# Kernel tuning notes

Hardware: AMD Instinct MI355X
Metric: run time of the kernel (lower is better)

Reference implementation:

```python
import jax, jax.numpy as jnp
import numpy as np

TOPK = 8
MIN_TEMP = 0.5
NEG = -1e9  # finite stand-in for -inf (same softmax result, safe grads)


def setup_inputs() -> dict:
    key = jax.random.key(0)
    ks = jax.random.split(key, 6)
    B, S, D, N, K = 4, 4096, 1024, 256, 8
    token_states = jax.random.normal(ks[0], (B, S, D), dtype=jnp.float32)
    set_states = jax.random.normal(ks[1], (B, N, D), dtype=jnp.float32)
    desc_router = jax.random.normal(ks[2], (N, D), dtype=jnp.float32)
    token_to_sets = jax.random.randint(ks[3], (S, K), 0, N)
    Wq = jax.random.normal(ks[4], (D, D), dtype=jnp.float32) / np.sqrt(D)
    bq = jnp.zeros((D,), dtype=jnp.float32)
    temperature = jnp.ones((1,), dtype=jnp.float32)
    return {"token_states": token_states, "set_states": set_states,
            "desc_router": desc_router, "token_to_sets": token_to_sets,
            "Wq": Wq, "bq": bq, "temperature": temperature}


def reference(token_states, set_states, desc_router, token_to_sets, Wq, bq, temperature):
    B, S, D = token_states.shape
    N = set_states.shape[1]
    scale = 1.0 / np.sqrt(D)

    # q = Linear(token_states)
    q = jnp.einsum('bsd,ed->bse', token_states, Wq) + bq
    scores = jnp.einsum('bse,ne->bsn', q, desc_router) * scale  # [B,S,N]

    # restrict_to_sets: boolean routing mask built by scatter
    rows = jnp.broadcast_to(jnp.arange(S)[:, None], token_to_sets.shape)
    cols = jnp.clip(token_to_sets, 0, N - 1)
    valid = token_to_sets >= 0
    mask = jnp.zeros((S, N), dtype=bool).at[rows, cols].max(valid)
    scores = jnp.where(mask[None], scores, NEG)

    # top-k keep (topk < num_sets)
    topk_scores, topk_idx = jax.lax.top_k(scores, TOPK)
    b_idx = jnp.arange(B)[:, None, None]
    s_idx = jnp.arange(S)[None, :, None]
    keep = jnp.full_like(scores, NEG).at[b_idx, s_idx, topk_idx].set(topk_scores)

    temp = jnp.maximum(temperature, MIN_TEMP)  # clamp(min=0.5)
    weights = jax.nn.softmax(keep / temp, axis=-1)  # [B,S,N]
    token_repr = jnp.einsum('bsn,bnd->bsd', weights, set_states)
    bank_indices = jnp.argmax(weights, axis=-1)
    return token_repr, bank_indices, weights, topk_idx
```

## Files before the change

### kernel.cpp

```cpp
#include <hip/hip_runtime.h>
#include <math.h>
#include <float.h>


namespace {
constexpr int kB = 4, kS = 4096, kD = 1024, kN = 256, kK = 8;
constexpr float kScale = 0.03125f;
constexpr float kNeg = -1e9f;
constexpr float kLog2e = 1.4426950408889634f;
constexpr size_t kBankOff = (size_t)kB * kS * kD;
constexpr size_t kWOff    = kBankOff + (size_t)kB * kS;
constexpr size_t kTopkOff = kWOff + (size_t)kB * kS * kN;
constexpr int kEC = 16;
constexpr int kEL = kD / kEC;
constexpr int kNT = kN / 8;
}

#if __has_builtin(__builtin_amdgcn_exp2f)
#define FAST_EXP2(x) __builtin_amdgcn_exp2f(x)
#else
#define FAST_EXP2(x) exp2f(x)
#endif
#if __has_builtin(__builtin_amdgcn_rcpf)
#define FAST_RCP(x) __builtin_amdgcn_rcpf(x)
#else
#define FAST_RCP(x) (1.0f / (x))
#endif

__global__ __launch_bounds__(256) void k_prep(const float* __restrict__ dr,
                                              const float* __restrict__ wq,
                                              float* __restrict__ part) {
  const int nt = blockIdx.x, ec = blockIdx.y, t = threadIdx.x;
  const float4* wq4 = reinterpret_cast<const float4*>(wq);
  float4 acc[8];
#pragma unroll
  for (int j = 0; j < 8; ++j) acc[j] = make_float4(0.f, 0.f, 0.f, 0.f);
  const int e0 = ec * kEL;
#pragma unroll 4
  for (int e = e0; e < e0 + kEL; ++e) {
    const float4 wv = wq4[(size_t)e * (kD / 4) + t];
#pragma unroll
    for (int j = 0; j < 8; ++j) {
      const float a = dr[(size_t)(nt * 8 + j) * kD + e];
      acc[j].x += a * wv.x; acc[j].y += a * wv.y;
      acc[j].z += a * wv.z; acc[j].w += a * wv.w;
    }
  }
  float4* p4 = reinterpret_cast<float4*>(part);
#pragma unroll
  for (int j = 0; j < 8; ++j)
    p4[((size_t)ec * kN + nt * 8 + j) * (kD / 4) + t] = acc[j];
}

__global__ __launch_bounds__(256) void k_reduce(const float* __restrict__ part,
                                                const float* __restrict__ dr,
                                                const float* __restrict__ bq,
                                                float* __restrict__ R,
                                                float* __restrict__ bias) {
  const int n = blockIdx.x, t = threadIdx.x;
  const float4* p4 = reinterpret_cast<const float4*>(part);
  float4 a = make_float4(0.f, 0.f, 0.f, 0.f);
#pragma unroll
  for (int ec = 0; ec < kEC; ++ec) {
    const float4 p = p4[((size_t)ec * kN + n) * (kD / 4) + t];
    a.x += p.x; a.y += p.y; a.z += p.z; a.w += p.w;
  }
  a.x *= kScale; a.y *= kScale; a.z *= kScale; a.w *= kScale;
  reinterpret_cast<float4*>(R)[(size_t)n * (kD / 4) + t] = a;

  if (t < 64) {
    const float4* b4 = reinterpret_cast<const float4*>(bq);
    const float4* dr4 = reinterpret_cast<const float4*>(dr + (size_t)n * kD);
    float p = 0.f;
#pragma unroll
    for (int i = 0; i < 4; ++i) {
      const float4 bb = b4[t * 4 + i];
      const float4 dd = dr4[t * 4 + i];
      p += bb.x * dd.x + bb.y * dd.y + bb.z * dd.z + bb.w * dd.w;
    }
#pragma unroll
    for (int off = 32; off; off >>= 1) p += __shfl_xor(p, off);
    if (t == 0) bias[n] = p * kScale;
  }
}

__global__ __launch_bounds__(256) void k_main(const float* __restrict__ ts,
                                              const float* __restrict__ ss,
                                              const int* __restrict__ t2s,
                                              const float* __restrict__ R,
                                              const float* __restrict__ bias,
                                              const float* __restrict__ temp_p,
                                              float* __restrict__ out) {
  const int lane = threadIdx.x & 63;
  const int wid = threadIdx.x >> 6;
  const int bid = blockIdx.x;
  const int xcd = bid & 7;
  const int b = xcd >> 1;
  int s_ = ((bid >> 3) << 2) + wid + ((xcd & 1) << 11);
  const int s = __builtin_amdgcn_readfirstlane(s_);
  const size_t row = (size_t)b * kS + s;

  int nraw[kK], nk[kK];
#pragma unroll
  for (int k = 0; k < kK; ++k) {
    nraw[k] = t2s[s * kK + k];
    const int n = nraw[k];
    nk[k] = n < 0 ? 0 : (n > kN - 1 ? kN - 1 : n);
  }
  int validmask = 0;
#pragma unroll
  for (int k = 0; k < kK; ++k) {
    bool v = (nraw[k] >= 0);
#pragma unroll
    for (int j = 0; j < kK; ++j)
      if (j < k && nk[j] == nk[k]) v = false;
    validmask |= v ? (1 << k) : 0;
  }
  const int cnt = __popc(validmask);

  const float4* ssb = reinterpret_cast<const float4*>(ss) + (size_t)b * kN * (kD / 4);
  float4 s0[kK];
#pragma unroll
  for (int k = 0; k < kK; ++k) s0[k] = ssb[(size_t)nk[k] * (kD / 4) + lane];

  const float4* t4 = reinterpret_cast<const float4*>(ts) + row * (kD / 4);
  const float4 tv0 = t4[lane];
  const float4 tv1 = t4[64 + lane];
  const float4 tv2 = t4[128 + lane];
  const float4 tv3 = t4[192 + lane];

  float pk[kK];
#pragma unroll
  for (int k = 0; k < kK; ++k) {
    const float4* r4 = reinterpret_cast<const float4*>(R) + (size_t)nk[k] * (kD / 4);
    const float4 r0 = r4[lane];
    const float4 r1 = r4[64 + lane];
    const float4 r2 = r4[128 + lane];
    const float4 r3 = r4[192 + lane];
    float a = tv0.x * r0.x + tv0.y * r0.y + tv0.z * r0.z + tv0.w * r0.w;
    a += tv1.x * r1.x + tv1.y * r1.y + tv1.z * r1.z + tv1.w * r1.w;
    a += tv2.x * r2.x + tv2.y * r2.y + tv2.z * r2.z + tv2.w * r2.w;
    a += tv3.x * r3.x + tv3.y * r3.y + tv3.z * r3.z + tv3.w * r3.w;
    pk[k] = a;
  }
#pragma unroll
  for (int k = 0; k < kK; ++k) {
    float a = pk[k];
    a += __shfl_xor(a, 1);
    a += __shfl_xor(a, 2);
    a += __shfl_xor(a, 4);
    a += __shfl_xor(a, 8);
    a += __shfl_xor(a, 16);
    a += __shfl_xor(a, 32);
    pk[k] = a + bias[nk[k]];
  }

  float mx = -INFINITY;
#pragma unroll
  for (int k = 0; k < kK; ++k)
    mx = fmaxf(mx, ((validmask >> k) & 1) ? pk[k] : -INFINITY);
  const float it = kLog2e * FAST_RCP(fmaxf(temp_p[0], 0.5f));
  float w[kK];
  float denom = 0.f;
#pragma unroll
  for (int k = 0; k < kK; ++k) {
    const float e = ((validmask >> k) & 1) ? FAST_EXP2((pk[k] - mx) * it) : 0.f;
    w[k] = e;
    denom += e;
  }
  const float rd = FAST_RCP(denom);
#pragma unroll
  for (int k = 0; k < kK; ++k) w[k] *= rd;

  float4* o4 = reinterpret_cast<float4*>(out) + row * (kD / 4);
  {
    float4 acc = make_float4(0.f, 0.f, 0.f, 0.f);
#pragma unroll
    for (int k = 0; k < kK; ++k) {
      acc.x += w[k] * s0[k].x; acc.y += w[k] * s0[k].y;
      acc.z += w[k] * s0[k].z; acc.w += w[k] * s0[k].w;
    }
    o4[lane] = acc;
  }
#pragma unroll
  for (int c = 1; c < 4; ++c) {
    float4 v[kK];
#pragma unroll
    for (int k = 0; k < kK; ++k)
      v[k] = ssb[(size_t)nk[k] * (kD / 4) + c * 64 + lane];
    float4 acc = make_float4(0.f, 0.f, 0.f, 0.f);
#pragma unroll
    for (int k = 0; k < kK; ++k) {
      acc.x += w[k] * v[k].x; acc.y += w[k] * v[k].y;
      acc.z += w[k] * v[k].z; acc.w += w[k] * v[k].w;
    }
    o4[c * 64 + lane] = acc;
  }

  {
    const int c0 = lane * 4;
    float4 wv = make_float4(0.f, 0.f, 0.f, 0.f);
#pragma unroll
    for (int k = 0; k < kK; ++k) {
      const bool vb = (validmask >> k) & 1;
      wv.x = (vb && nk[k] == c0    ) ? w[k] : wv.x;
      wv.y = (vb && nk[k] == c0 + 1) ? w[k] : wv.y;
      wv.z = (vb && nk[k] == c0 + 2) ? w[k] : wv.z;
      wv.w = (vb && nk[k] == c0 + 3) ? w[k] : wv.w;
    }
    reinterpret_cast<float4*>(out + kWOff)[row * (kN / 4) + lane] = wv;
  }

  unsigned long long pm0 = 0, pm1 = 0, pm2 = 0, pm3 = 0;
#pragma unroll
  for (int k = 0; k < kK; ++k) {
    const bool v = (validmask >> k) & 1;
    const unsigned long long bit = 1ull << (nk[k] & 63);
    const int wd = nk[k] >> 6;
    pm0 |= (v && wd == 0) ? bit : 0ull;
    pm1 |= (v && wd == 1) ? bit : 0ull;
    pm2 |= (v && wd == 2) ? bit : 0ull;
    pm3 |= (v && wd == 3) ? bit : 0ull;
  }
  int seq[kK];
#pragma unroll
  for (int i = 0; i < kK; ++i) {
    const unsigned long long i0 = ~pm0, i1 = ~pm1, i2 = ~pm2, i3 = ~pm3;
    const int c = i0 ? (__ffsll(i0) - 1)
                     : (i1 ? 64 + (__ffsll(i1) - 1)
                           : (i2 ? 128 + (__ffsll(i2) - 1)
                                 : 192 + (__ffsll(i3) - 1)));
    seq[i] = c;
    const unsigned long long b2 = 1ull << (c & 63);
    const int wd = c >> 6;
    pm0 |= (wd == 0) ? b2 : 0ull;
    pm1 |= (wd == 1) ? b2 : 0ull;
    pm2 |= (wd == 2) ? b2 : 0ull;
    pm3 |= (wd == 3) ? b2 : 0ull;
  }

  float fs[kK];
  int fi[kK];
#pragma unroll
  for (int k = 0; k < kK; ++k) {
    const bool v = (validmask >> k) & 1;
    const int jk = __popc((~validmask) & ((1 << k) - 1));
    int fv = seq[0];
#pragma unroll
    for (int j = 1; j < kK; ++j) fv = (jk == j) ? seq[j] : fv;
    fs[k] = v ? pk[k] : kNeg;
    fi[k] = v ? nk[k] : fv;
  }
#define CE(A, B)                                                        \
  {                                                                     \
    const bool sw = (fs[B] > fs[A]) || (fs[B] == fs[A] && fi[B] < fi[A]); \
    const float fa = fs[A], fb = fs[B];                                 \
    const int ia = fi[A], ib = fi[B];                                   \
    fs[A] = sw ? fb : fa; fs[B] = sw ? fa : fb;                         \
    fi[A] = sw ? ib : ia; fi[B] = sw ? ia : ib;                         \
  }
  CE(0,1) CE(2,3) CE(4,5) CE(6,7)
  CE(0,2) CE(1,3) CE(4,6) CE(5,7)
  CE(1,2) CE(5,6)
  CE(0,4) CE(1,5) CE(2,6) CE(3,7)
  CE(2,4) CE(3,5)
  CE(1,2) CE(3,4) CE(5,6)
#undef CE

  if (lane < kK) {
    int v = fi[0];
#pragma unroll
    for (int k = 1; k < kK; ++k) v = (lane == k) ? fi[k] : v;
    out[kTopkOff + row * kK + lane] = (float)v;
  }
  if (lane == 0) out[kBankOff + row] = (float)fi[0];
}

extern "C" void kernel_launch(void* const* d_in, const int* in_sizes, int n_in,
                              void* d_out, int out_size, void* d_ws, size_t ws_size,
                              hipStream_t stream) {
  const float* ts  = (const float*)d_in[0];
  const float* ss  = (const float*)d_in[1];
  const float* dr  = (const float*)d_in[2];
  const int*   t2s = (const int*)  d_in[3];
  const float* wq  = (const float*)d_in[4];
  const float* bq  = (const float*)d_in[5];
  const float* tmp = (const float*)d_in[6];
  float* out = (float*)d_out;

  float* R    = (float*)d_ws;
  float* bias = R + (size_t)kN * kD;
  float* part = out + kWOff;

  k_prep<<<dim3(kNT, kEC), 256, 0, stream>>>(dr, wq, part);
  k_reduce<<<kN, 256, 0, stream>>>(part, dr, bq, R, bias);
  k_main<<<kB * kS / 4, 256, 0, stream>>>(ts, ss, t2s, R, bias, tmp, out);
}
```

Measured before the change: 71.08 us.

## Share routed R rows across batches via LDS, one block per token

Remaps k_main so each block handles one sequence position and its four waves handle the four batches. Those waves share the same token_to_sets routing, so the eight projected router rows are loaded once into shared memory and reused instead of being re-read from global memory per batch. Also software-pipelines the set_states gathers in chunks, moves the weights store earlier, sets launch_bounds occupancy to 3 blocks, and halves the split count in the prep kernel. In exchange it adds a block barrier and 32KB of LDS per block, which may limit occupancy.

```diff
diff --git a/kernel.cpp b/kernel.cpp
--- a/kernel.cpp
+++ b/kernel.cpp
@@ -11,7 +11,7 @@
 constexpr size_t kBankOff = (size_t)kB * kS * kD;
 constexpr size_t kWOff    = kBankOff + (size_t)kB * kS;
 constexpr size_t kTopkOff = kWOff + (size_t)kB * kS * kN;
-constexpr int kEC = 16;
+constexpr int kEC = 8;
 constexpr int kEL = kD / kEC;
 constexpr int kNT = kN / 8;
 }
@@ -84,21 +84,19 @@
   }
 }
 
-__global__ __launch_bounds__(256) void k_main(const float* __restrict__ ts,
-                                              const float* __restrict__ ss,
-                                              const int* __restrict__ t2s,
-                                              const float* __restrict__ R,
-                                              const float* __restrict__ bias,
-                                              const float* __restrict__ temp_p,
-                                              float* __restrict__ out) {
+__global__ __launch_bounds__(256, 3) void k_main(const float* __restrict__ ts,
+                                                 const float* __restrict__ ss,
+                                                 const int* __restrict__ t2s,
+                                                 const float* __restrict__ R,
+                                                 const float* __restrict__ bias,
+                                                 const float* __restrict__ temp_p,
+                                                 float* __restrict__ out) {
   const int lane = threadIdx.x & 63;
-  const int wid = threadIdx.x >> 6;
+  const int wvb = threadIdx.x >> 6;
   const int bid = blockIdx.x;
-  const int xcd = bid & 7;
-  const int b = xcd >> 1;
-  int s_ = ((bid >> 3) << 2) + wid + ((xcd & 1) << 11);
-  const int s = __builtin_amdgcn_readfirstlane(s_);
-  const size_t row = (size_t)b * kS + s;
+  const int s = __builtin_amdgcn_readfirstlane(((bid & 7) << 9) | (bid >> 3));
+
+  __shared__ float4 lr[kK * 256];
 
   int nraw[kK], nk[kK];
 #pragma unroll
@@ -116,27 +114,41 @@
       if (j < k && nk[j] == nk[k]) v = false;
     validmask |= v ? (1 << k) : 0;
   }
-  const int cnt = __popc(validmask);
-
-  const float4* ssb = reinterpret_cast<const float4*>(ss) + (size_t)b * kN * (kD / 4);
-  float4 s0[kK];
-#pragma unroll
-  for (int k = 0; k < kK; ++k) s0[k] = ssb[(size_t)nk[k] * (kD / 4) + lane];
-
+
+  {
+    const int rk = threadIdx.x >> 5, rc = threadIdx.x & 31;
+    int myrow = nk[0];
+#pragma unroll
+    for (int k = 1; k < kK; ++k) myrow = (rk == k) ? nk[k] : myrow;
+    const float4* R4 = reinterpret_cast<const float4*>(R);
+#pragma unroll
+    for (int j = 0; j < 8; ++j)
+      lr[rk * 256 + rc + 32 * j] = R4[(size_t)myrow * 256 + rc + 32 * j];
+  }
+
+  const float4* ssb = reinterpret_cast<const float4*>(ss) + (size_t)wvb * kN * (kD / 4);
+  float4 c0[kK], c1[kK];
+#pragma unroll
+  for (int k = 0; k < kK; ++k) c0[k] = ssb[(size_t)nk[k] * (kD / 4) + lane];
+#pragma unroll
+  for (int k = 0; k < kK; ++k) c1[k] = ssb[(size_t)nk[k] * (kD / 4) + 64 + lane];
+
+  const size_t row = (size_t)wvb * kS + s;
   const float4* t4 = reinterpret_cast<const float4*>(ts) + row * (kD / 4);
   const float4 tv0 = t4[lane];
   const float4 tv1 = t4[64 + lane];
   const float4 tv2 = t4[128 + lane];
   const float4 tv3 = t4[192 + lane];
 
+  __syncthreads();
+
   float pk[kK];
 #pragma unroll
   for (int k = 0; k < kK; ++k) {
-    const float4* r4 = reinterpret_cast<const float4*>(R) + (size_t)nk[k] * (kD / 4);
-    const float4 r0 = r4[lane];
-    const float4 r1 = r4[64 + lane];
-    const float4 r2 = r4[128 + lane];
-    const float4 r3 = r4[192 + lane];
+    const float4 r0 = lr[k * 256 + lane];
+    const float4 r1 = lr[k * 256 + 64 + lane];
+    const float4 r2 = lr[k * 256 + 128 + lane];
+    const float4 r3 = lr[k * 256 + 192 + lane];
     float a = tv0.x * r0.x + tv0.y * r0.y + tv0.z * r0.z + tv0.w * r0.w;
     a += tv1.x * r1.x + tv1.y * r1.y + tv1.z * r1.z + tv1.w * r1.w;
     a += tv2.x * r2.x + tv2.y * r2.y + tv2.z * r2.z + tv2.w * r2.w;
@@ -172,43 +184,62 @@
 #pragma unroll
   for (int k = 0; k < kK; ++k) w[k] *= rd;
 
+  {
+    const int cb = lane * 4;
+    float4 wvv = make_float4(0.f, 0.f, 0.f, 0.f);
+#pragma unroll
+    for (int k = 0; k < kK; ++k) {
+      const bool vb = (validmask >> k) & 1;
+      wvv.x = (vb && nk[k] == cb    ) ? w[k] : wvv.x;
+      wvv.y = (vb && nk[k] == cb + 1) ? w[k] : wvv.y;
+      wvv.z = (vb && nk[k] == cb + 2) ? w[k] : wvv.z;
+      wvv.w = (vb && nk[k] == cb + 3) ? w[k] : wvv.w;
+    }
+    reinterpret_cast<float4*>(out + kWOff)[row * (kN / 4) + lane] = wvv;
+  }
+
   float4* o4 = reinterpret_cast<float4*>(out) + row * (kD / 4);
   {
     float4 acc = make_float4(0.f, 0.f, 0.f, 0.f);
 #pragma unroll
     for (int k = 0; k < kK; ++k) {
-      acc.x += w[k] * s0[k].x; acc.y += w[k] * s0[k].y;
-      acc.z += w[k] * s0[k].z; acc.w += w[k] * s0[k].w;
+      acc.x += w[k] * c0[k].x; acc.y += w[k] * c0[k].y;
+      acc.z += w[k] * c0[k].z; acc.w += w[k] * c0[k].w;
     }
     o4[lane] = acc;
   }
-#pragma unroll
-  for (int c = 1; c < 4; ++c) {
-    float4 v[kK];
-#pragma unroll
-    for (int k = 0; k < kK; ++k)
-      v[k] = ssb[(size_t)nk[k] * (kD / 4) + c * 64 + lane];
+  float4 c2[kK];
+#pragma unroll
+  for (int k = 0; k < kK; ++k) c2[k] = ssb[(size_t)nk[k] * (kD / 4) + 128 + lane];
+  {
     float4 acc = make_float4(0.f, 0.f, 0.f, 0.f);
 #pragma unroll
     for (int k = 0; k < kK; ++k) {
-      acc.x += w[k] * v[k].x; acc.y += w[k] * v[k].y;
-      acc.z += w[k] * v[k].z; acc.w += w[k] * v[k].w;
-    }
-    o4[c * 64 + lane] = acc;
-  }
-
-  {
-    const int c0 = lane * 4;
-    float4 wv = make_float4(0.f, 0.f, 0.f, 0.f);
-#pragma unroll
-    for (int k = 0; k < kK; ++k) {
-      const bool vb = (validmask >> k) & 1;
-      wv.x = (vb && nk[k] == c0    ) ? w[k] : wv.x;
-      wv.y = (vb && nk[k] == c0 + 1) ? w[k] : wv.y;
-      wv.z = (vb && nk[k] == c0 + 2) ? w[k] : wv.z;
-      wv.w = (vb && nk[k] == c0 + 3) ? w[k] : wv.w;
-    }
-    reinterpret_cast<float4*>(out + kWOff)[row * (kN / 4) + lane] = wv;
+      acc.x += w[k] * c1[k].x; acc.y += w[k] * c1[k].y;
+      acc.z += w[k] * c1[k].z; acc.w += w[k] * c1[k].w;
+    }
+    o4[64 + lane] = acc;
+  }
+  float4 c3[kK];
+#pragma unroll
+  for (int k = 0; k < kK; ++k) c3[k] = ssb[(size_t)nk[k] * (kD / 4) + 192 + lane];
+  {
+    float4 acc = make_float4(0.f, 0.f, 0.f, 0.f);
+#pragma unroll
+    for (int k = 0; k < kK; ++k) {
+      acc.x += w[k] * c2[k].x; acc.y += w[k] * c2[k].y;
+      acc.z += w[k] * c2[k].z; acc.w += w[k] * c2[k].w;
+    }
+    o4[128 + lane] = acc;
+  }
+  {
+    float4 acc = make_float4(0.f, 0.f, 0.f, 0.f);
+#pragma unroll
+    for (int k = 0; k < kK; ++k) {
+      acc.x += w[k] * c3[k].x; acc.y += w[k] * c3[k].y;
+      acc.z += w[k] * c3[k].z; acc.w += w[k] * c3[k].w;
+    }
+    o4[192 + lane] = acc;
   }
 
   unsigned long long pm0 = 0, pm1 = 0, pm2 = 0, pm3 = 0;
@@ -294,5 +325,5 @@
 
   k_prep<<<dim3(kNT, kEC), 256, 0, stream>>>(dr, wq, part);
   k_reduce<<<kN, 256, 0, stream>>>(part, dr, bq, R, bias);
-  k_main<<<kB * kS / 4, 256, 0, stream>>>(ts, ss, t2s, R, bias, tmp, out);
-}
+  k_main<<<kS, 256, 0, stream>>>(ts, ss, t2s, R, bias, tmp, out);
+}
```

New measurement: 87.14 us. +22.6%, slower.

## Split main kernel into scoring and weighted-gather kernels, halve prep split

Applied to the files above, without the earlier changes.

Splits the fused kernel into a scoring/top-k kernel that writes per-row weights and sorted indices to workspace, and a second kernel that gathers set_states and writes token_repr and the dense weights. This lowers register pressure in each kernel so more waves can hide memory latency. The softmax is now computed over the sorted top-k entries. It also halves the k_prep split factor. In exchange it adds a kernel launch and a small workspace round trip.

```diff
diff --git a/kernel.cpp b/kernel.cpp
--- a/kernel.cpp
+++ b/kernel.cpp
@@ -11,7 +11,7 @@
 constexpr size_t kBankOff = (size_t)kB * kS * kD;
 constexpr size_t kWOff    = kBankOff + (size_t)kB * kS;
 constexpr size_t kTopkOff = kWOff + (size_t)kB * kS * kN;
-constexpr int kEC = 16;
+constexpr int kEC = 8;
 constexpr int kEL = kD / kEC;
 constexpr int kNT = kN / 8;
 }
@@ -84,13 +84,13 @@
   }
 }
 
-__global__ __launch_bounds__(256) void k_main(const float* __restrict__ ts,
-                                              const float* __restrict__ ss,
-                                              const int* __restrict__ t2s,
-                                              const float* __restrict__ R,
-                                              const float* __restrict__ bias,
-                                              const float* __restrict__ temp_p,
-                                              float* __restrict__ out) {
+__global__ __launch_bounds__(256) void k_score(const float* __restrict__ ts,
+                                               const int* __restrict__ t2s,
+                                               const float* __restrict__ R,
+                                               const float* __restrict__ bias,
+                                               const float* __restrict__ temp_p,
+                                               int* __restrict__ st,
+                                               float* __restrict__ out) {
   const int lane = threadIdx.x & 63;
   const int wid = threadIdx.x >> 6;
   const int bid = blockIdx.x;
@@ -117,11 +117,6 @@
     validmask |= v ? (1 << k) : 0;
   }
   const int cnt = __popc(validmask);
-
-  const float4* ssb = reinterpret_cast<const float4*>(ss) + (size_t)b * kN * (kD / 4);
-  float4 s0[kK];
-#pragma unroll
-  for (int k = 0; k < kK; ++k) s0[k] = ssb[(size_t)nk[k] * (kD / 4) + lane];
 
   const float4* t4 = reinterpret_cast<const float4*>(ts) + row * (kD / 4);
   const float4 tv0 = t4[lane];
@@ -153,62 +148,6 @@
     a += __shfl_xor(a, 16);
     a += __shfl_xor(a, 32);
     pk[k] = a + bias[nk[k]];
-  }
-
-  float mx = -INFINITY;
-#pragma unroll
-  for (int k = 0; k < kK; ++k)
-    mx = fmaxf(mx, ((validmask >> k) & 1) ? pk[k] : -INFINITY);
-  const float it = kLog2e * FAST_RCP(fmaxf(temp_p[0], 0.5f));
-  float w[kK];
-  float denom = 0.f;
-#pragma unroll
-  for (int k = 0; k < kK; ++k) {
-    const float e = ((validmask >> k) & 1) ? FAST_EXP2((pk[k] - mx) * it) : 0.f;
-    w[k] = e;
-    denom += e;
-  }
-  const float rd = FAST_RCP(denom);
-#pragma unroll
-  for (int k = 0; k < kK; ++k) w[k] *= rd;
-
-  float4* o4 = reinterpret_cast<float4*>(out) + row * (kD / 4);
-  {
-    float4 acc = make_float4(0.f, 0.f, 0.f, 0.f);
-#pragma unroll
-    for (int k = 0; k < kK; ++k) {
-      acc.x += w[k] * s0[k].x; acc.y += w[k] * s0[k].y;
-      acc.z += w[k] * s0[k].z; acc.w += w[k] * s0[k].w;
-    }
-    o4[lane] = acc;
-  }
-#pragma unroll
-  for (int c = 1; c < 4; ++c) {
-    float4 v[kK];
-#pragma unroll
-    for (int k = 0; k < kK; ++k)
-      v[k] = ssb[(size_t)nk[k] * (kD / 4) + c * 64 + lane];
-    float4 acc = make_float4(0.f, 0.f, 0.f, 0.f);
-#pragma unroll
-    for (int k = 0; k < kK; ++k) {
-      acc.x += w[k] * v[k].x; acc.y += w[k] * v[k].y;
-      acc.z += w[k] * v[k].z; acc.w += w[k] * v[k].w;
-    }
-    o4[c * 64 + lane] = acc;
-  }
-
-  {
-    const int c0 = lane * 4;
-    float4 wv = make_float4(0.f, 0.f, 0.f, 0.f);
-#pragma unroll
-    for (int k = 0; k < kK; ++k) {
-      const bool vb = (validmask >> k) & 1;
-      wv.x = (vb && nk[k] == c0    ) ? w[k] : wv.x;
-      wv.y = (vb && nk[k] == c0 + 1) ? w[k] : wv.y;
-      wv.z = (vb && nk[k] == c0 + 2) ? w[k] : wv.z;
-      wv.w = (vb && nk[k] == c0 + 3) ? w[k] : wv.w;
-    }
-    reinterpret_cast<float4*>(out + kWOff)[row * (kN / 4) + lane] = wv;
   }
 
   unsigned long long pm0 = 0, pm1 = 0, pm2 = 0, pm3 = 0;
@@ -267,6 +206,19 @@
   CE(1,2) CE(3,4) CE(5,6)
 #undef CE
 
+  const float it = kLog2e * FAST_RCP(fmaxf(temp_p[0], 0.5f));
+  float w[kK];
+  float denom = 0.f;
+#pragma unroll
+  for (int i = 0; i < kK; ++i) {
+    const float e = (i < cnt) ? FAST_EXP2((fs[i] - fs[0]) * it) : 0.f;
+    w[i] = e;
+    denom += e;
+  }
+  const float rd = FAST_RCP(denom);
+#pragma unroll
+  for (int i = 0; i < kK; ++i) w[i] *= rd;
+
   if (lane < kK) {
     int v = fi[0];
 #pragma unroll
@@ -274,6 +226,72 @@
     out[kTopkOff + row * kK + lane] = (float)v;
   }
   if (lane == 0) out[kBankOff + row] = (float)fi[0];
+
+  int sel = 0;
+#pragma unroll
+  for (int k = 0; k < kK; ++k) {
+    sel = (lane == k) ? __float_as_int(w[k]) : sel;
+    sel = (lane == k + kK) ? fi[k] : sel;
+  }
+  if (lane < 16) st[row * 16 + lane] = sel;
+}
+
+__global__ __launch_bounds__(256) void k_repr(const float* __restrict__ ss,
+                                              const int* __restrict__ st,
+                                              float* __restrict__ out) {
+  const int lane = threadIdx.x & 63;
+  const int wid = threadIdx.x >> 6;
+  const int bid = blockIdx.x;
+  const int xcd = bid & 7;
+  const int b = xcd >> 1;
+  int s_ = ((bid >> 3) << 2) + wid + ((xcd & 1) << 11);
+  const int s = __builtin_amdgcn_readfirstlane(s_);
+  const size_t row = (size_t)b * kS + s;
+
+  float w[kK];
+  int fi[kK];
+#pragma unroll
+  for (int k = 0; k < kK; ++k) {
+    w[k] = __int_as_float(st[row * 16 + k]);
+    fi[k] = st[row * 16 + kK + k];
+  }
+
+  const float4* ssb = reinterpret_cast<const float4*>(ss) + (size_t)b * kN * (kD / 4);
+  float4* o4 = reinterpret_cast<float4*>(out) + row * (kD / 4);
+#pragma unroll
+  for (int c = 0; c < 4; ++c) {
+    float4 v0 = ssb[(size_t)fi[0] * (kD / 4) + c * 64 + lane];
+    float4 v1 = ssb[(size_t)fi[1] * (kD / 4) + c * 64 + lane];
+    float4 v2 = ssb[(size_t)fi[2] * (kD / 4) + c * 64 + lane];
+    float4 v3 = ssb[(size_t)fi[3] * (kD / 4) + c * 64 + lane];
+    float4 v4 = ssb[(size_t)fi[4] * (kD / 4) + c * 64 + lane];
+    float4 v5 = ssb[(size_t)fi[5] * (kD / 4) + c * 64 + lane];
+    float4 v6 = ssb[(size_t)fi[6] * (kD / 4) + c * 64 + lane];
+    float4 v7 = ssb[(size_t)fi[7] * (kD / 4) + c * 64 + lane];
+    float4 acc;
+    acc.x = w[0] * v0.x + w[1] * v1.x + w[2] * v2.x + w[3] * v3.x
+          + w[4] * v4.x + w[5] * v5.x + w[6] * v6.x + w[7] * v7.x;
+    acc.y = w[0] * v0.y + w[1] * v1.y + w[2] * v2.y + w[3] * v3.y
+          + w[4] * v4.y + w[5] * v5.y + w[6] * v6.y + w[7] * v7.y;
+    acc.z = w[0] * v0.z + w[1] * v1.z + w[2] * v2.z + w[3] * v3.z
+          + w[4] * v4.z + w[5] * v5.z + w[6] * v6.z + w[7] * v7.z;
+    acc.w = w[0] * v0.w + w[1] * v1.w + w[2] * v2.w + w[3] * v3.w
+          + w[4] * v4.w + w[5] * v5.w + w[6] * v6.w + w[7] * v7.w;
+    o4[c * 64 + lane] = acc;
+  }
+
+  {
+    const int cb = lane * 4;
+    float4 wv = make_float4(0.f, 0.f, 0.f, 0.f);
+#pragma unroll
+    for (int k = 0; k < kK; ++k) {
+      wv.x = (fi[k] == cb    ) ? w[k] : wv.x;
+      wv.y = (fi[k] == cb + 1) ? w[k] : wv.y;
+      wv.z = (fi[k] == cb + 2) ? w[k] : wv.z;
+      wv.w = (fi[k] == cb + 3) ? w[k] : wv.w;
+    }
+    reinterpret_cast<float4*>(out + kWOff)[row * (kN / 4) + lane] = wv;
+  }
 }
 
 extern "C" void kernel_launch(void* const* d_in, const int* in_sizes, int n_in,
@@ -290,9 +308,11 @@
 
   float* R    = (float*)d_ws;
   float* bias = R + (size_t)kN * kD;
+  int*   st   = (int*)(bias + kN);
   float* part = out + kWOff;
 
   k_prep<<<dim3(kNT, kEC), 256, 0, stream>>>(dr, wq, part);
   k_reduce<<<kN, 256, 0, stream>>>(part, dr, bq, R, bias);
-  k_main<<<kB * kS / 4, 256, 0, stream>>>(ts, ss, t2s, R, bias, tmp, out);
-}
+  k_score<<<kB * kS / 4, 256, 0, stream>>>(ts, t2s, R, bias, tmp, st, out);
+  k_repr<<<kB * kS / 4, 256, 0, stream>>>(ss, st, out);
+}
```

Result: slower. 81.27 us (+14.3%).
